# Performance work log

Hardware: AMD Instinct MI355X
Metric: run time of the kernel (lower is better)

The kernel has to match this reference:

```python
import jax, jax.numpy as jnp
import numpy as np

NEG_SLOPE = 0.2  # PyG GATConv default


def gat_conv(x, src, dst, W_src, W_dst, a_src, a_dst, b):
    """PyG GATConv with concat=False (mean over heads) and bias.
    x: [N, F_in]; src/dst: [E]; W_*: [F_in, H*D]; a_*: [H, D]; b: [D]."""
    N = x.shape[0]
    H, D = a_src.shape
    hs = (x @ W_src).reshape(N, H, D)
    hd = (x @ W_dst).reshape(N, H, D)
    al_s = (hs * a_src).sum(-1)  # [N, H]
    al_d = (hd * a_dst).sum(-1)  # [N, H]
    logits = jax.nn.leaky_relu(al_s[src] + al_d[dst], NEG_SLOPE)  # [E, H]
    # segment softmax over incoming edges of each dst node
    m = jax.lax.stop_gradient(jax.ops.segment_max(logits, dst, num_segments=N))
    e = jnp.exp(logits - m[dst])
    denom = jax.ops.segment_sum(e, dst, num_segments=N)  # [N, H]
    alpha = e / denom[dst]  # [E, H]
    msg = alpha[:, :, None] * hs[src]  # [E, H, D]
    out = jax.ops.segment_sum(msg, dst, num_segments=N)  # [N, H, D]
    return out.mean(axis=1) + b  # concat=False -> mean over heads


def setup_inputs() -> dict:
    key = jax.random.key(0)
    ks = jax.random.split(key, 12)
    N, F, Dh, H, E = 100000, 128, 128, 1, 1600000
    s = 0.05
    return {
        "x": jax.random.normal(ks[0], (N, F), jnp.float32),
        "edge_index": jax.random.randint(ks[1], (2, E), 0, N, jnp.int32),
        "W1_src": jax.random.normal(ks[2], (F, H * Dh), jnp.float32) * s,
        "W1_dst": jax.random.normal(ks[3], (F, H * Dh), jnp.float32) * s,
        "a1_src": jax.random.normal(ks[4], (H, Dh), jnp.float32) * s,
        "a1_dst": jax.random.normal(ks[5], (H, Dh), jnp.float32) * s,
        "b1": jnp.zeros((Dh,), jnp.float32),
        "W2_src": jax.random.normal(ks[6], (Dh, H * Dh), jnp.float32) * s,
        "W2_dst": jax.random.normal(ks[7], (Dh, H * Dh), jnp.float32) * s,
        "a2_src": jax.random.normal(ks[8], (H, Dh), jnp.float32) * s,
        "a2_dst": jax.random.normal(ks[9], (H, Dh), jnp.float32) * s,
        "b2": jnp.zeros((Dh,), jnp.float32),
    }


def reference(x, edge_index, W1_src, W1_dst, a1_src, a1_dst, b1,
              W2_src, W2_dst, a2_src, a2_dst, b2):
    src, dst = edge_index[0], edge_index[1]
    h = gat_conv(x, src, dst, W1_src, W1_dst, a1_src, a1_dst, b1)
    h = jax.nn.relu(h)  # ReLU between layers, none after the last
    out = gat_conv(h, src, dst, W2_src, W2_dst, a2_src, a2_dst, b2)
    return out
```

## Files before the change

kernel.cpp:

```cpp
#include <hip/hip_runtime.h>
#include <hip/hip_bf16.h>
#include <hip/hip_fp16.h>
#include <math.h>
#include <type_traits>


#define BKT_SHIFT 8
#define MAX_NB 512
#define EPB 2048

typedef _Float16 half8 __attribute__((ext_vector_type(8)));
typedef float floatx4 __attribute__((ext_vector_type(4)));

__global__ void convert_w_kernel(const float* __restrict__ W1,
                                 const float* __restrict__ W2,
                                 __half* __restrict__ wt1,
                                 __half* __restrict__ wt2) {
    const float* W = (blockIdx.x >> 4) ? W2 : W1;
    __half* WT = (blockIdx.x >> 4) ? wt2 : wt1;
    const int sub = blockIdx.x & 15;
    const int k0 = (sub >> 2) * 32, c0 = (sub & 3) * 32;
    __shared__ float t[32][33];
    const int r = threadIdx.x >> 5, c = threadIdx.x & 31;
    for (int rr = r; rr < 32; rr += 8)
        t[rr][c] = W[(size_t)(k0 + rr) * 128 + c0 + c];
    __syncthreads();
    for (int rr = r; rr < 32; rr += 8)
        WT[(size_t)(c0 + rr) * 128 + k0 + c] = __float2half_rn(t[c][rr]);
}

__global__ void make_wv4_kernel(const float* __restrict__ W1s,
                                const float* __restrict__ a1s,
                                const float* __restrict__ W1d,
                                const float* __restrict__ a1d,
                                const float* __restrict__ W2s,
                                const float* __restrict__ a2s,
                                const float* __restrict__ W2d,
                                const float* __restrict__ a2d,
                                float* __restrict__ wv) {
    const float* Wt[4] = {W1s, W1d, W2s, W2d};
    const float* at[4] = {a1s, a1d, a2s, a2d};
    const float* W = Wt[blockIdx.x];
    const float* a = at[blockIdx.x];
    int k = threadIdx.x;
    float s = 0.f;
    for (int d = 0; d < 128; ++d) s += W[k * 128 + d] * a[d];
    wv[blockIdx.x * 128 + k] = s;
}

template <typename InT>
__global__ void compute_al_kernel(const InT* __restrict__ X,
                                  const float* __restrict__ wsv,
                                  const float* __restrict__ wdv,
                                  float* __restrict__ al_s,
                                  float* __restrict__ al_d, int N) {
    int node = (int)((blockIdx.x * (unsigned)blockDim.x + threadIdx.x) >> 6);
    int lane = threadIdx.x & 63;
    if (node >= N) return;
    float2 xv;
    if constexpr (std::is_same<InT, float>::value) {
        xv = *(const float2*)&X[(size_t)node * 128 + lane * 2];
    } else {
        xv = __half22float2(*(const __half2*)&X[(size_t)node * 128 + lane * 2]);
    }
    float2 sv = *(const float2*)&wsv[lane * 2];
    float2 dv = *(const float2*)&wdv[lane * 2];
    float ps = xv.x * sv.x + xv.y * sv.y;
    float pd = xv.x * dv.x + xv.y * dv.y;
    for (int o = 32; o >= 1; o >>= 1) {
        ps += __shfl_xor(ps, o);
        pd += __shfl_xor(pd, o);
    }
    if (lane == 0) { al_s[node] = ps; al_d[node] = pd; }
}

__global__ void bucket_count_kernel(const int* __restrict__ dst,
                                    int* __restrict__ counts, int E, int NB) {
    __shared__ int h[MAX_NB];
    for (int i = threadIdx.x; i < NB; i += 256) h[i] = 0;
    __syncthreads();
    const int base = blockIdx.x * EPB;
#pragma unroll
    for (int j = 0; j < EPB / 256; ++j) {
        int i = base + j * 256 + threadIdx.x;
        if (i < E) atomicAdd(&h[dst[i] >> BKT_SHIFT], 1);
    }
    __syncthreads();
    for (int i = threadIdx.x; i < NB; i += 256)
        counts[(size_t)blockIdx.x * NB + i] = h[i];
}

__global__ void bucket_prefix_kernel(int* __restrict__ counts,
                                     int* __restrict__ totals, int NBLK,
                                     int NB) {
    __shared__ int lsum[256];
    const int b = blockIdx.x;
    const int t = threadIdx.x;
    int v[4];
    const int base = t * 4;
#pragma unroll
    for (int k = 0; k < 4; ++k) {
        int blk = base + k;
        v[k] = (blk < NBLK) ? counts[(size_t)blk * NB + b] : 0;
    }
    int s = v[0] + v[1] + v[2] + v[3];
    lsum[t] = s;
    __syncthreads();
    for (int o = 1; o < 256; o <<= 1) {
        int u = (t >= o) ? lsum[t - o] : 0;
        __syncthreads();
        lsum[t] += u;
        __syncthreads();
    }
    int run = lsum[t] - s;
#pragma unroll
    for (int k = 0; k < 4; ++k) {
        int blk = base + k;
        if (blk < NBLK) counts[(size_t)blk * NB + b] = run;
        run += v[k];
    }
    if (t == 255) totals[b] = lsum[255];
}

__global__ void bucket_base_kernel(const int* __restrict__ totals,
                                   int* __restrict__ bbase, int NB) {
    __shared__ int sh[MAX_NB];
    int t = threadIdx.x;
    int v = (t < NB) ? totals[t] : 0;
    sh[t] = v;
    __syncthreads();
    for (int o = 1; o < MAX_NB; o <<= 1) {
        int u = (t >= o) ? sh[t - o] : 0;
        __syncthreads();
        sh[t] += u;
        __syncthreads();
    }
    if (t < NB) bbase[t] = sh[t] - v;
}

__global__ void bucket_place_kernel(const int* __restrict__ src,
                                    const int* __restrict__ dst,
                                    const int* __restrict__ prefix,
                                    const int* __restrict__ bbase,
                                    int* __restrict__ bpack, int E, int NB) {
    __shared__ int cur[MAX_NB];
    const int blk = blockIdx.x;
    for (int i = threadIdx.x; i < NB; i += 256)
        cur[i] = bbase[i] + prefix[(size_t)blk * NB + i];
    __syncthreads();
    const int base = blk * EPB;
#pragma unroll
    for (int j = 0; j < EPB / 256; ++j) {
        int i = base + j * 256 + threadIdx.x;
        if (i < E) {
            int d = dst[i], s = src[i];
            int p = atomicAdd(&cur[d >> BKT_SHIFT], 1);
            bpack[p] = ((d & 255) << 17) | s;
        }
    }
}

__global__ void bucket_csr_kernel(const int* __restrict__ bpack,
                                  const int* __restrict__ bbase,
                                  int* __restrict__ row_ptr,
                                  int* __restrict__ col, int N, int E,
                                  int NB) {
    __shared__ int cnt[256];
    __shared__ int cur[256];
    const int b = blockIdx.x;
    const int t = threadIdx.x;
    const int node0 = b << BKT_SHIFT;
    const int s = bbase[b];
    const int e = (b + 1 < NB) ? bbase[b + 1] : E;
    cnt[t] = 0;
    __syncthreads();
    for (int i = s + t; i < e; i += 256) atomicAdd(&cnt[bpack[i] >> 17], 1);
    __syncthreads();
    int v = cnt[t];
    cur[t] = v;
    __syncthreads();
    for (int o = 1; o < 256; o <<= 1) {
        int u = (t >= o) ? cur[t - o] : 0;
        __syncthreads();
        cur[t] += u;
        __syncthreads();
    }
    int start = cur[t] - v;
    if (node0 + t < N) row_ptr[node0 + t] = s + start;
    __syncthreads();
    cur[t] = s + start;
    __syncthreads();
    for (int i = s + t; i < e; i += 256) {
        int pk = bpack[i];
        int p = atomicAdd(&cur[pk >> 17], 1);
        col[p] = pk & 0x1FFFF;
    }
    if (b == 0 && t == 0) row_ptr[N] = E;
}

template <typename InT>
__global__ __launch_bounds__(256) void gemm_mfma_kernel(
    const InT* __restrict__ X, const __half* __restrict__ WT,
    __half* __restrict__ C, int N) {
    __shared__ __align__(16) __half Ws[128][136];
    __shared__ __align__(16) __half Xs[64][136];
    const int tid = threadIdx.x;
    const int row0 = blockIdx.x * 64;

    {
        int cr = tid >> 1, off = (tid & 1) * 64;
        const __half* srcp = &WT[(size_t)cr * 128 + off];
#pragma unroll
        for (int q = 0; q < 8; ++q)
            *(float4*)&Ws[cr][off + q * 8] = *(const float4*)&srcp[q * 8];
    }
    {
        int xr = tid >> 2, co = (tid & 3) * 32;
        int gr = row0 + xr;
        if constexpr (std::is_same<InT, float>::value) {
#pragma unroll
            for (int q = 0; q < 4; ++q) {
                float4 lo = make_float4(0.f, 0.f, 0.f, 0.f);
                float4 hi = make_float4(0.f, 0.f, 0.f, 0.f);
                if (gr < N) {
                    lo = *(const float4*)&X[(size_t)gr * 128 + co + q * 8];
                    hi = *(const float4*)&X[(size_t)gr * 128 + co + q * 8 + 4];
                }
                __align__(16) __half2 tmp[4];
                tmp[0] = __floats2half2_rn(lo.x, lo.y);
                tmp[1] = __floats2half2_rn(lo.z, lo.w);
                tmp[2] = __floats2half2_rn(hi.x, hi.y);
                tmp[3] = __floats2half2_rn(hi.z, hi.w);
                *(float4*)&Xs[xr][co + q * 8] = *(const float4*)tmp;
            }
        } else {
#pragma unroll
            for (int q = 0; q < 4; ++q) {
                float4 vz = make_float4(0.f, 0.f, 0.f, 0.f);
                if (gr < N)
                    vz = *(const float4*)&X[(size_t)gr * 128 + co + q * 8];
                *(float4*)&Xs[xr][co + q * 8] = vz;
            }
        }
    }
    __syncthreads();

    const int wid = tid >> 6;
    const int lane = tid & 63;
    const int lr = lane & 15, ks = lane >> 4;
    floatx4 acc[8];
#pragma unroll
    for (int t = 0; t < 8; ++t) acc[t] = (floatx4){0.f, 0.f, 0.f, 0.f};

#pragma unroll
    for (int kk = 0; kk < 4; ++kk) {
        half8 a = *(const half8*)&Xs[wid * 16 + lr][kk * 32 + ks * 8];
#pragma unroll
        for (int t = 0; t < 8; ++t) {
            half8 b = *(const half8*)&Ws[t * 16 + lr][kk * 32 + ks * 8];
            acc[t] = __builtin_amdgcn_mfma_f32_16x16x32_f16(a, b, acc[t], 0, 0, 0);
        }
    }
#pragma unroll
    for (int r = 0; r < 4; ++r) {
        int grow = row0 + wid * 16 + ks * 4 + r;
        if (grow < N) {
#pragma unroll
            for (int t = 0; t < 8; ++t)
                C[(size_t)grow * 128 + t * 16 + lr] = __float2half_rn(acc[t][r]);
        }
    }
}

template <typename OutT, bool RELU>
__global__ __launch_bounds__(256) void gat_aggregate_fused(
    const __half* __restrict__ hs, const float* __restrict__ al_s,
    const float* __restrict__ al_d, const int* __restrict__ row_ptr,
    const int* __restrict__ col, const float* __restrict__ bias,
    OutT* __restrict__ out, int N) {
    int node = (int)((blockIdx.x * 256u + threadIdx.x) >> 6);
    int lane = threadIdx.x & 63;
    if (node >= N) return;
    const int begin = row_ptr[node], end = row_ptr[node + 1];
    const float ald = al_d[node];
    const int d0 = lane * 2;

    float acc0 = 0.f, acc1 = 0.f, den = 0.f;
    for (int base = begin; base < end; base += 64) {
        const int cnt = min(64, end - base);
        int myidx = 0;
        float w = 0.f;
        if (lane < cnt) {
            myidx = col[base + lane];
            float l = al_s[myidx] + ald;
            l = (l >= 0.f) ? l : 0.2f * l;
            w = __expf(l);
        }
        float ws = w;
#pragma unroll
        for (int o = 32; o >= 1; o >>= 1) ws += __shfl_xor(ws, o);
        den += ws;

        for (int e = 0; e < cnt; e += 8) {
            __half2 v[8];
            float we[8];
#pragma unroll
            for (int j = 0; j < 8; ++j) {
                int s = __shfl(myidx, e + j);
                we[j] = __shfl(w, e + j);
                v[j] = *(const __half2*)&hs[((size_t)(unsigned)s << 7) + d0];
            }
#pragma unroll
            for (int j = 0; j < 8; ++j) {
                float2 f = __half22float2(v[j]);
                acc0 = fmaf(we[j], f.x, acc0);
                acc1 = fmaf(we[j], f.y, acc1);
            }
        }
    }
    const float rden = (den > 0.f) ? 1.f / den : 0.f;
    float o0 = acc0 * rden + bias[d0];
    float o1 = acc1 * rden + bias[d0 + 1];
    if (RELU) { o0 = fmaxf(o0, 0.f); o1 = fmaxf(o1, 0.f); }
    if constexpr (std::is_same<OutT, __half>::value) {
        *(__half2*)&out[(size_t)node * 128 + d0] = __floats2half2_rn(o0, o1);
    } else {
        *(float2*)&out[(size_t)node * 128 + d0] = make_float2(o0, o1);
    }
}

extern "C" void kernel_launch(void* const* d_in, const int* in_sizes, int n_in,
                              void* d_out, int out_size, void* d_ws,
                              size_t ws_size, hipStream_t stream) {
    const float* x    = (const float*)d_in[0];
    const int*  eidx  = (const int*)d_in[1];
    const float* W1s  = (const float*)d_in[2];
    const float* W1d  = (const float*)d_in[3];
    const float* a1s  = (const float*)d_in[4];
    const float* a1d  = (const float*)d_in[5];
    const float* b1   = (const float*)d_in[6];
    const float* W2s  = (const float*)d_in[7];
    const float* W2d  = (const float*)d_in[8];
    const float* a2s  = (const float*)d_in[9];
    const float* a2d  = (const float*)d_in[10];
    const float* b2   = (const float*)d_in[11];

    const int N = in_sizes[0] / 128;
    const int E = in_sizes[1] / 2;
    const int* src = eidx;
    const int* dst = eidx + E;

    const int NB   = (N + 255) >> BKT_SHIFT;
    const int NBLK = (E + EPB - 1) / EPB;

    char* p = (char*)d_ws;
    auto alloc = [&](size_t bytes) {
        char* r = p;
        p += (bytes + 255) & ~(size_t)255;
        return r;
    };
    __half* hsA   = (__half*)alloc((size_t)N * 128 * 2);
    __half* h1    = (__half*)alloc((size_t)N * 128 * 2);
    int*   row_ptr= (int*)alloc((size_t)(N + 1) * 4);
    int*   col    = (int*)alloc((size_t)E * 4);
    int*   bpack  = (int*)alloc((size_t)E * 4);
    int*   counts = (int*)alloc((size_t)NBLK * NB * 4);
    int*   totals = (int*)alloc(MAX_NB * 4);
    int*   bbase  = (int*)alloc(MAX_NB * 4);
    float* al_s   = (float*)alloc((size_t)N * 4);
    float* al_d   = (float*)alloc((size_t)N * 4);
    float* wv     = (float*)alloc(4 * 128 * 4);
    __half* wt1   = (__half*)alloc(128 * 128 * 2);
    __half* wt2   = (__half*)alloc(128 * 128 * 2);

    convert_w_kernel<<<32, 256, 0, stream>>>(W1s, W2s, wt1, wt2);
    make_wv4_kernel<<<4, 128, 0, stream>>>(W1s, a1s, W1d, a1d, W2s, a2s, W2d,
                                           a2d, wv);

    bucket_count_kernel<<<NBLK, 256, 0, stream>>>(dst, counts, E, NB);
    bucket_prefix_kernel<<<NB, 256, 0, stream>>>(counts, totals, NBLK, NB);
    bucket_base_kernel<<<1, MAX_NB, 0, stream>>>(totals, bbase, NB);
    bucket_place_kernel<<<NBLK, 256, 0, stream>>>(src, dst, counts, bbase,
                                                  bpack, E, NB);
    bucket_csr_kernel<<<NB, 256, 0, stream>>>(bpack, bbase, row_ptr, col, N, E,
                                              NB);

    const int gemm_grid = (N + 63) / 64;
    const int wave_grid = (N + 3) / 4;

    gemm_mfma_kernel<float><<<gemm_grid, 256, 0, stream>>>(x, wt1, hsA, N);
    compute_al_kernel<float><<<wave_grid, 256, 0, stream>>>(
        x, wv + 0, wv + 128, al_s, al_d, N);
    gat_aggregate_fused<__half, true><<<wave_grid, 256, 0, stream>>>(
        hsA, al_s, al_d, row_ptr, col, b1, h1, N);

    gemm_mfma_kernel<__half><<<gemm_grid, 256, 0, stream>>>(h1, wt2, hsA, N);
    compute_al_kernel<__half><<<wave_grid, 256, 0, stream>>>(
        h1, wv + 256, wv + 384, al_s, al_d, N);
    gat_aggregate_fused<float, false><<<wave_grid, 256, 0, stream>>>(
        hsA, al_s, al_d, row_ptr, col, b2, (float*)d_out, N);
}
```

Measured before the change: 262.2 us.

## Fuse attention-logit dot products into GEMM and precompute edge weights in separate pass

Removes the standalone compute_al kernel by computing the node attention scores inside the MFMA GEMM epilogue from the X tile already in shared memory. Adds a per-edge destination-id array in CSR construction and a new edge_weight kernel that computes exp(leaky_relu) weights into packed (col, weight) pairs, so aggregation no longer does random al_s gathers on its critical path. This trades an extra edge pass and extra E*12 bytes of traffic per layer for simpler aggregation. X is rounded to half in the epilogue, which slightly changes precision for layer one.

Result: slower. 281.4 us (+7.3%).

```diff
diff --git a/kernel.cpp b/kernel.cpp
--- a/kernel.cpp
+++ b/kernel.cpp
@@ -48,32 +48,6 @@
     wv[blockIdx.x * 128 + k] = s;
 }
 
-template <typename InT>
-__global__ void compute_al_kernel(const InT* __restrict__ X,
-                                  const float* __restrict__ wsv,
-                                  const float* __restrict__ wdv,
-                                  float* __restrict__ al_s,
-                                  float* __restrict__ al_d, int N) {
-    int node = (int)((blockIdx.x * (unsigned)blockDim.x + threadIdx.x) >> 6);
-    int lane = threadIdx.x & 63;
-    if (node >= N) return;
-    float2 xv;
-    if constexpr (std::is_same<InT, float>::value) {
-        xv = *(const float2*)&X[(size_t)node * 128 + lane * 2];
-    } else {
-        xv = __half22float2(*(const __half2*)&X[(size_t)node * 128 + lane * 2]);
-    }
-    float2 sv = *(const float2*)&wsv[lane * 2];
-    float2 dv = *(const float2*)&wdv[lane * 2];
-    float ps = xv.x * sv.x + xv.y * sv.y;
-    float pd = xv.x * dv.x + xv.y * dv.y;
-    for (int o = 32; o >= 1; o >>= 1) {
-        ps += __shfl_xor(ps, o);
-        pd += __shfl_xor(pd, o);
-    }
-    if (lane == 0) { al_s[node] = ps; al_d[node] = pd; }
-}
-
 __global__ void bucket_count_kernel(const int* __restrict__ dst,
                                     int* __restrict__ counts, int E, int NB) {
     __shared__ int h[MAX_NB];
@@ -163,7 +137,8 @@
 __global__ void bucket_csr_kernel(const int* __restrict__ bpack,
                                   const int* __restrict__ bbase,
                                   int* __restrict__ row_ptr,
-                                  int* __restrict__ col, int N, int E,
+                                  int* __restrict__ col,
+                                  int* __restrict__ dstid, int N, int E,
                                   int NB) {
     __shared__ int cnt[256];
     __shared__ int cur[256];
@@ -192,16 +167,48 @@
     __syncthreads();
     for (int i = s + t; i < e; i += 256) {
         int pk = bpack[i];
-        int p = atomicAdd(&cur[pk >> 17], 1);
+        int d = pk >> 17;
+        int p = atomicAdd(&cur[d], 1);
         col[p] = pk & 0x1FFFF;
+        dstid[p] = node0 + d;
     }
     if (b == 0 && t == 0) row_ptr[N] = E;
+}
+
+__global__ void edge_weight_kernel(const int* __restrict__ col,
+                                   const int* __restrict__ dstid,
+                                   const float* __restrict__ al_s,
+                                   const float* __restrict__ al_d,
+                                   int2* __restrict__ wpack, int E) {
+    const int base = blockIdx.x * 1024;
+    const int t = threadIdx.x;
+    int c[4], d[4];
+    bool ok[4];
+#pragma unroll
+    for (int j = 0; j < 4; ++j) {
+        int i = base + j * 256 + t;
+        ok[j] = (i < E);
+        c[j] = ok[j] ? col[i] : 0;
+        d[j] = ok[j] ? dstid[i] : 0;
+    }
+    float l[4];
+#pragma unroll
+    for (int j = 0; j < 4; ++j) l[j] = al_s[c[j]] + al_d[d[j]];
+#pragma unroll
+    for (int j = 0; j < 4; ++j) {
+        float ll = (l[j] >= 0.f) ? l[j] : 0.2f * l[j];
+        float w = __expf(ll);
+        int i = base + j * 256 + t;
+        if (ok[j]) wpack[i] = make_int2(c[j], __float_as_int(w));
+    }
 }
 
 template <typename InT>
 __global__ __launch_bounds__(256) void gemm_mfma_kernel(
     const InT* __restrict__ X, const __half* __restrict__ WT,
-    __half* __restrict__ C, int N) {
+    __half* __restrict__ C, const float* __restrict__ wvs,
+    const float* __restrict__ wvd, float* __restrict__ al_s,
+    float* __restrict__ al_d, int N) {
     __shared__ __align__(16) __half Ws[128][136];
     __shared__ __align__(16) __half Xs[64][136];
     const int tid = threadIdx.x;
@@ -270,19 +277,33 @@
                 C[(size_t)grow * 128 + t * 16 + lr] = __float2half_rn(acc[t][r]);
         }
     }
+
+    {
+        const int r = tid >> 2, q = tid & 3;
+        float ps = 0.f, pd = 0.f;
+        const int dbase = q * 32;
+#pragma unroll
+        for (int d = 0; d < 32; ++d) {
+            float xv = __half2float(Xs[r][dbase + d]);
+            ps = fmaf(xv, wvs[dbase + d], ps);
+            pd = fmaf(xv, wvd[dbase + d], pd);
+        }
+        ps += __shfl_xor(ps, 1); ps += __shfl_xor(ps, 2);
+        pd += __shfl_xor(pd, 1); pd += __shfl_xor(pd, 2);
+        int gr = row0 + r;
+        if (q == 0 && gr < N) { al_s[gr] = ps; al_d[gr] = pd; }
+    }
 }
 
 template <typename OutT, bool RELU>
 __global__ __launch_bounds__(256) void gat_aggregate_fused(
-    const __half* __restrict__ hs, const float* __restrict__ al_s,
-    const float* __restrict__ al_d, const int* __restrict__ row_ptr,
-    const int* __restrict__ col, const float* __restrict__ bias,
+    const __half* __restrict__ hs, const int2* __restrict__ wpack,
+    const int* __restrict__ row_ptr, const float* __restrict__ bias,
     OutT* __restrict__ out, int N) {
     int node = (int)((blockIdx.x * 256u + threadIdx.x) >> 6);
     int lane = threadIdx.x & 63;
     if (node >= N) return;
     const int begin = row_ptr[node], end = row_ptr[node + 1];
-    const float ald = al_d[node];
     const int d0 = lane * 2;
 
     float acc0 = 0.f, acc1 = 0.f, den = 0.f;
@@ -291,10 +312,9 @@
         int myidx = 0;
         float w = 0.f;
         if (lane < cnt) {
-            myidx = col[base + lane];
-            float l = al_s[myidx] + ald;
-            l = (l >= 0.f) ? l : 0.2f * l;
-            w = __expf(l);
+            int2 pw = wpack[base + lane];
+            myidx = pw.x;
+            w = __int_as_float(pw.y);
         }
         float ws = w;
 #pragma unroll
@@ -363,6 +383,8 @@
     __half* h1    = (__half*)alloc((size_t)N * 128 * 2);
     int*   row_ptr= (int*)alloc((size_t)(N + 1) * 4);
     int*   col    = (int*)alloc((size_t)E * 4);
+    int*   dstid  = (int*)alloc((size_t)E * 4);
+    int2*  wpack  = (int2*)alloc((size_t)E * 8);
     int*   bpack  = (int*)alloc((size_t)E * 4);
     int*   counts = (int*)alloc((size_t)NBLK * NB * 4);
     int*   totals = (int*)alloc(MAX_NB * 4);
@@ -382,21 +404,24 @@
     bucket_base_kernel<<<1, MAX_NB, 0, stream>>>(totals, bbase, NB);
     bucket_place_kernel<<<NBLK, 256, 0, stream>>>(src, dst, counts, bbase,
                                                   bpack, E, NB);
-    bucket_csr_kernel<<<NB, 256, 0, stream>>>(bpack, bbase, row_ptr, col, N, E,
-                                              NB);
+    bucket_csr_kernel<<<NB, 256, 0, stream>>>(bpack, bbase, row_ptr, col,
+                                              dstid, N, E, NB);
 
     const int gemm_grid = (N + 63) / 64;
     const int wave_grid = (N + 3) / 4;
-
-    gemm_mfma_kernel<float><<<gemm_grid, 256, 0, stream>>>(x, wt1, hsA, N);
-    compute_al_kernel<float><<<wave_grid, 256, 0, stream>>>(
-        x, wv + 0, wv + 128, al_s, al_d, N);
+    const int ew_grid   = (E + 1023) / 1024;
+
+    gemm_mfma_kernel<float><<<gemm_grid, 256, 0, stream>>>(
+        x, wt1, hsA, wv + 0, wv + 128, al_s, al_d, N);
+    edge_weight_kernel<<<ew_grid, 256, 0, stream>>>(col, dstid, al_s, al_d,
+                                                    wpack, E);
     gat_aggregate_fused<__half, true><<<wave_grid, 256, 0, stream>>>(
-        hsA, al_s, al_d, row_ptr, col, b1, h1, N);
-
-    gemm_mfma_kernel<__half><<<gemm_grid, 256, 0, stream>>>(h1, wt2, hsA, N);
-    compute_al_kernel<__half><<<wave_grid, 256, 0, stream>>>(
-        h1, wv + 256, wv + 384, al_s, al_d, N);
+        hsA, wpack, row_ptr, b1, h1, N);
+
+    gemm_mfma_kernel<__half><<<gemm_grid, 256, 0, stream>>>(
+        h1, wt2, hsA, wv + 256, wv + 384, al_s, al_d, N);
+    edge_weight_kernel<<<ew_grid, 256, 0, stream>>>(col, dstid, al_s, al_d,
+                                                    wpack, E);
     gat_aggregate_fused<float, false><<<wave_grid, 256, 0, stream>>>(
-        hsA, al_s, al_d, row_ptr, col, b2, (float*)d_out, N);
-}
+        hsA, wpack, row_ptr, b2, (float*)d_out, N);
+}
```

## Fuse attention logit dot-products into GEMM and merge weight prep kernels

Applied to the files above, without the earlier changes.

The per-node attention scalars al_s/al_d are now computed inside the MFMA GEMM epilogue from the X tile already staged in shared memory. This removes two separate kernels that re-read the node features from global memory. The two weight-preparation kernels are merged into one launch. The aggregation gather is unrolled to 16 edges per batch for more loads in flight. The fused path computes layer-1 logits from fp16-rounded x, which slightly changes precision, and the larger unroll raises register pressure.

Result: faster. 245.7 us (-6.3%).

```diff
diff --git a/kernel.cpp b/kernel.cpp
--- a/kernel.cpp
+++ b/kernel.cpp
@@ -12,66 +12,40 @@
 typedef _Float16 half8 __attribute__((ext_vector_type(8)));
 typedef float floatx4 __attribute__((ext_vector_type(4)));
 
-__global__ void convert_w_kernel(const float* __restrict__ W1,
-                                 const float* __restrict__ W2,
-                                 __half* __restrict__ wt1,
-                                 __half* __restrict__ wt2) {
-    const float* W = (blockIdx.x >> 4) ? W2 : W1;
-    __half* WT = (blockIdx.x >> 4) ? wt2 : wt1;
-    const int sub = blockIdx.x & 15;
-    const int k0 = (sub >> 2) * 32, c0 = (sub & 3) * 32;
-    __shared__ float t[32][33];
-    const int r = threadIdx.x >> 5, c = threadIdx.x & 31;
-    for (int rr = r; rr < 32; rr += 8)
-        t[rr][c] = W[(size_t)(k0 + rr) * 128 + c0 + c];
-    __syncthreads();
-    for (int rr = r; rr < 32; rr += 8)
-        WT[(size_t)(c0 + rr) * 128 + k0 + c] = __float2half_rn(t[c][rr]);
-}
-
-__global__ void make_wv4_kernel(const float* __restrict__ W1s,
-                                const float* __restrict__ a1s,
-                                const float* __restrict__ W1d,
-                                const float* __restrict__ a1d,
-                                const float* __restrict__ W2s,
-                                const float* __restrict__ a2s,
-                                const float* __restrict__ W2d,
-                                const float* __restrict__ a2d,
-                                float* __restrict__ wv) {
-    const float* Wt[4] = {W1s, W1d, W2s, W2d};
-    const float* at[4] = {a1s, a1d, a2s, a2d};
-    const float* W = Wt[blockIdx.x];
-    const float* a = at[blockIdx.x];
-    int k = threadIdx.x;
-    float s = 0.f;
-    for (int d = 0; d < 128; ++d) s += W[k * 128 + d] * a[d];
-    wv[blockIdx.x * 128 + k] = s;
-}
-
-template <typename InT>
-__global__ void compute_al_kernel(const InT* __restrict__ X,
-                                  const float* __restrict__ wsv,
-                                  const float* __restrict__ wdv,
-                                  float* __restrict__ al_s,
-                                  float* __restrict__ al_d, int N) {
-    int node = (int)((blockIdx.x * (unsigned)blockDim.x + threadIdx.x) >> 6);
-    int lane = threadIdx.x & 63;
-    if (node >= N) return;
-    float2 xv;
-    if constexpr (std::is_same<InT, float>::value) {
-        xv = *(const float2*)&X[(size_t)node * 128 + lane * 2];
-    } else {
-        xv = __half22float2(*(const __half2*)&X[(size_t)node * 128 + lane * 2]);
-    }
-    float2 sv = *(const float2*)&wsv[lane * 2];
-    float2 dv = *(const float2*)&wdv[lane * 2];
-    float ps = xv.x * sv.x + xv.y * sv.y;
-    float pd = xv.x * dv.x + xv.y * dv.y;
-    for (int o = 32; o >= 1; o >>= 1) {
-        ps += __shfl_xor(ps, o);
-        pd += __shfl_xor(pd, o);
-    }
-    if (lane == 0) { al_s[node] = ps; al_d[node] = pd; }
+__global__ void prep_kernel(const float* __restrict__ W1s,
+                            const float* __restrict__ a1s,
+                            const float* __restrict__ W1d,
+                            const float* __restrict__ a1d,
+                            const float* __restrict__ W2s,
+                            const float* __restrict__ a2s,
+                            const float* __restrict__ W2d,
+                            const float* __restrict__ a2d,
+                            __half* __restrict__ wt1,
+                            __half* __restrict__ wt2,
+                            float* __restrict__ wv) {
+    if (blockIdx.x < 32) {
+        const float* W = (blockIdx.x >> 4) ? W2s : W1s;
+        __half* WT = (blockIdx.x >> 4) ? wt2 : wt1;
+        const int sub = blockIdx.x & 15;
+        const int k0 = (sub >> 2) * 32, c0 = (sub & 3) * 32;
+        __shared__ float t[32][33];
+        const int r = threadIdx.x >> 5, c = threadIdx.x & 31;
+        for (int rr = r; rr < 32; rr += 8)
+            t[rr][c] = W[(size_t)(k0 + rr) * 128 + c0 + c];
+        __syncthreads();
+        for (int rr = r; rr < 32; rr += 8)
+            WT[(size_t)(c0 + rr) * 128 + k0 + c] = __float2half_rn(t[c][rr]);
+    } else if (threadIdx.x < 128) {
+        const float* Wt[4] = {W1s, W1d, W2s, W2d};
+        const float* at[4] = {a1s, a1d, a2s, a2d};
+        const int b = blockIdx.x - 32;
+        const float* W = Wt[b];
+        const float* a = at[b];
+        int k = threadIdx.x;
+        float s = 0.f;
+        for (int d = 0; d < 128; ++d) s += W[k * 128 + d] * a[d];
+        wv[b * 128 + k] = s;
+    }
 }
 
 __global__ void bucket_count_kernel(const int* __restrict__ dst,
@@ -201,7 +175,9 @@
 template <typename InT>
 __global__ __launch_bounds__(256) void gemm_mfma_kernel(
     const InT* __restrict__ X, const __half* __restrict__ WT,
-    __half* __restrict__ C, int N) {
+    __half* __restrict__ C, const float* __restrict__ wvs,
+    const float* __restrict__ wvd, float* __restrict__ al_s,
+    float* __restrict__ al_d, int N) {
     __shared__ __align__(16) __half Ws[128][136];
     __shared__ __align__(16) __half Xs[64][136];
     const int tid = threadIdx.x;
@@ -270,6 +246,22 @@
                 C[(size_t)grow * 128 + t * 16 + lr] = __float2half_rn(acc[t][r]);
         }
     }
+
+    {
+        const int r = tid >> 2, q = tid & 3;
+        float ps = 0.f, pd = 0.f;
+        const int dbase = q * 32;
+#pragma unroll
+        for (int d = 0; d < 32; ++d) {
+            float xv = __half2float(Xs[r][dbase + d]);
+            ps = fmaf(xv, wvs[dbase + d], ps);
+            pd = fmaf(xv, wvd[dbase + d], pd);
+        }
+        ps += __shfl_xor(ps, 1); ps += __shfl_xor(ps, 2);
+        pd += __shfl_xor(pd, 1); pd += __shfl_xor(pd, 2);
+        int gr = row0 + r;
+        if (q == 0 && gr < N) { al_s[gr] = ps; al_d[gr] = pd; }
+    }
 }
 
 template <typename OutT, bool RELU>
@@ -301,17 +293,17 @@
         for (int o = 32; o >= 1; o >>= 1) ws += __shfl_xor(ws, o);
         den += ws;
 
-        for (int e = 0; e < cnt; e += 8) {
-            __half2 v[8];
-            float we[8];
-#pragma unroll
-            for (int j = 0; j < 8; ++j) {
+        for (int e = 0; e < cnt; e += 16) {
+            __half2 v[16];
+            float we[16];
+#pragma unroll
+            for (int j = 0; j < 16; ++j) {
                 int s = __shfl(myidx, e + j);
                 we[j] = __shfl(w, e + j);
                 v[j] = *(const __half2*)&hs[((size_t)(unsigned)s << 7) + d0];
             }
 #pragma unroll
-            for (int j = 0; j < 8; ++j) {
+            for (int j = 0; j < 16; ++j) {
                 float2 f = __half22float2(v[j]);
                 acc0 = fmaf(we[j], f.x, acc0);
                 acc1 = fmaf(we[j], f.y, acc1);
@@ -373,9 +365,8 @@
     __half* wt1   = (__half*)alloc(128 * 128 * 2);
     __half* wt2   = (__half*)alloc(128 * 128 * 2);
 
-    convert_w_kernel<<<32, 256, 0, stream>>>(W1s, W2s, wt1, wt2);
-    make_wv4_kernel<<<4, 128, 0, stream>>>(W1s, a1s, W1d, a1d, W2s, a2s, W2d,
-                                           a2d, wv);
+    prep_kernel<<<36, 256, 0, stream>>>(W1s, a1s, W1d, a1d, W2s, a2s, W2d,
+                                        a2d, wt1, wt2, wv);
 
     bucket_count_kernel<<<NBLK, 256, 0, stream>>>(dst, counts, E, NB);
     bucket_prefix_kernel<<<NB, 256, 0, stream>>>(counts, totals, NBLK, NB);
@@ -388,15 +379,13 @@
     const int gemm_grid = (N + 63) / 64;
     const int wave_grid = (N + 3) / 4;
 
-    gemm_mfma_kernel<float><<<gemm_grid, 256, 0, stream>>>(x, wt1, hsA, N);
-    compute_al_kernel<float><<<wave_grid, 256, 0, stream>>>(
-        x, wv + 0, wv + 128, al_s, al_d, N);
+    gemm_mfma_kernel<float><<<gemm_grid, 256, 0, stream>>>(
+        x, wt1, hsA, wv + 0, wv + 128, al_s, al_d, N);
     gat_aggregate_fused<__half, true><<<wave_grid, 256, 0, stream>>>(
         hsA, al_s, al_d, row_ptr, col, b1, h1, N);
 
-    gemm_mfma_kernel<__half><<<gemm_grid, 256, 0, stream>>>(h1, wt2, hsA, N);
-    compute_al_kernel<__half><<<wave_grid, 256, 0, stream>>>(
-        h1, wv + 256, wv + 384, al_s, al_d, N);
+    gemm_mfma_kernel<__half><<<gemm_grid, 256, 0, stream>>>(
+        h1, wt2, hsA, wv + 256, wv + 384, al_s, al_d, N);
     gat_aggregate_fused<float, false><<<wave_grid, 256, 0, stream>>>(
         hsA, al_s, al_d, row_ptr, col, b2, (float*)d_out, N);
 }
```
